# Kernel tuning notes

Measured on AMD Instinct MI355X. Metric: run time of the kernel, lower is better.

## Reference

```python
import jax, jax.numpy as jnp
import numpy as np

K = 4       # wavelet basis size
C = 4       # wavelet channels
ALPHA = 64  # retained Fourier modes per SparseKernelFT
L = 0       # coarsest-level cutoff


def setup_inputs() -> dict:
    key = jax.random.key(0)
    ks = jax.random.split(key, 14)
    B, N = 32, 16384
    ck = C * K
    wscale = 1.0 / (ck * ck)  # matches torch.rand(...)/in_ch^2 scale

    def cw(k1, k2):
        return (jax.random.normal(k1, (ck, ck, ALPHA), jnp.float32) * wscale,
                jax.random.normal(k2, (ck, ck, ALPHA), jnp.float32) * wscale)

    wA_re, wA_im = cw(ks[1], ks[2])
    wB_re, wB_im = cw(ks[3], ks[4])
    wC_re, wC_im = cw(ks[5], ks[6])
    fs = 1.0 / np.sqrt(2.0 * K)  # stand-in scale for orthonormal Legendre filter banks
    return {
        "x": jax.random.normal(ks[0], (B, N, C, K), jnp.float32),
        "ec_s": jax.random.normal(ks[7], (2 * K, K), jnp.float32) * fs,
        "ec_d": jax.random.normal(ks[8], (2 * K, K), jnp.float32) * fs,
        "rc_e": jax.random.normal(ks[9], (2 * K, K), jnp.float32) * fs,
        "rc_o": jax.random.normal(ks[10], (2 * K, K), jnp.float32) * fs,
        "t0_w": jax.random.normal(ks[11], (K, K), jnp.float32) / np.sqrt(K),
        "t0_b": jnp.zeros((K,), jnp.float32),
        "wA_re": wA_re, "wA_im": wA_im,
        "wB_re": wB_re, "wB_im": wB_im,
        "wC_re": wC_re, "wC_im": wC_im,
    }


def _sparse_ft(x, w_re, w_im):
    # SparseKernelFT (1D): rfft -> truncated-mode complex mixing -> irfft.
    B, N, c, k = x.shape
    ck = c * k
    xr = x.reshape(B, N, ck).transpose(0, 2, 1)        # (B, ck, N)
    xf = jnp.fft.rfft(xr)                               # (B, ck, N//2+1)
    nf = N // 2 + 1
    l = min(ALPHA, nf)
    w = (w_re + 1j * w_im)[:, :, :l]                    # (ck, ck, l) complex
    out = jnp.einsum('bix,iox->box', xf[:, :, :l], w)
    out_full = jnp.zeros((B, ck, nf), dtype=out.dtype).at[:, :, :l].set(out)
    y = jnp.fft.irfft(out_full, n=N)                    # real (B, ck, N)
    return y.transpose(0, 2, 1).reshape(B, N, c, k)


def _forward(x, ec_s, ec_d, rc_e, rc_o, t0_w, t0_b,
             wA_re, wA_im, wB_re, wB_im, wC_re, wC_im):
    B, N, c, k = x.shape
    ns = int(np.log2(N))
    Ud, Us = [], []
    # decomposition: N -> N/2 -> ... -> 2^L
    for _ in range(ns - L):
        xa = jnp.concatenate([x[:, ::2], x[:, 1::2]], axis=-1)  # (B, n/2, c, 2k)
        d = xa @ ec_d   # detail coefficients
        x = xa @ ec_s   # scale coefficients
        Ud.append(_sparse_ft(d, wA_re, wA_im) + _sparse_ft(x, wB_re, wB_im))
        Us.append(_sparse_ft(d, wC_re, wC_im))
    # coarsest-scale linear map T0 over last dim k
    x = x @ t0_w.T + t0_b
    # reconstruction with even/odd interleaving
    for i in range(ns - 1 - L, -1, -1):
        x = x + Us[i]
        xc = jnp.concatenate([x, Ud[i]], axis=-1)   # (B, n, c, 2k)
        x_e = xc @ rc_e                              # (B, n, c, k)
        x_o = xc @ rc_o
        b, n = x_e.shape[0], x_e.shape[1]
        x = jnp.stack([x_e, x_o], axis=2).reshape(b, 2 * n, c, k)
    return x


def reference(x, ec_s, ec_d, rc_e, rc_o, t0_w, t0_b,
              wA_re, wA_im, wB_re, wB_im, wC_re, wC_im):
    return _forward(x, ec_s, ec_d, rc_e, rc_o, t0_w, t0_b,
                    wA_re, wA_im, wB_re, wB_im, wC_re, wC_im)
```

## Files before the change

### kernel.cpp

```cpp
#include <hip/hip_runtime.h>

#define TWO_PI 6.28318530717958647692f

constexpr int BB   = 32;
constexpr int NTOT = 16384;
constexpr int CKd  = 16;
constexpr int NLEV = 14;

__device__ __forceinline__ void decomp_row(const float* __restrict__ src,
                                           const float* __restrict__ ec_s,
                                           const float* __restrict__ ec_d,
                                           float* d, float* s)
{
  float xa[32];
#pragma unroll
  for (int q = 0; q < 8; ++q) {
    float4 v = reinterpret_cast<const float4*>(src)[q];
    xa[q*4+0] = v.x; xa[q*4+1] = v.y; xa[q*4+2] = v.z; xa[q*4+3] = v.w;
  }
#pragma unroll
  for (int c = 0; c < 4; ++c) {
#pragma unroll
    for (int j = 0; j < 4; ++j) {
      float ad = 0.f, as = 0.f;
#pragma unroll
      for (int m = 0; m < 4; ++m) {
        const float xe = xa[c*4+m];
        const float xo = xa[16+c*4+m];
        ad += xe * ec_d[m*4+j] + xo * ec_d[(4+m)*4+j];
        as += xe * ec_s[m*4+j] + xo * ec_s[(4+m)*4+j];
      }
      d[c*4+j] = ad; s[c*4+j] = as;
    }
  }
}

__global__ __launch_bounds__(256) void fwd_big(
    const float* __restrict__ xin, float* __restrict__ xout,
    float* __restrict__ Fd, float* __restrict__ Fx,
    const float* __restrict__ ec_s, const float* __restrict__ ec_d,
    int nhalf)
{
  __shared__ float smem[16384];
  float* Pd = smem;
  float* Md = smem + 4096;
  float* Ps = smem + 8192;
  float* Ms = smem + 12288;
  const int b    = blockIdx.x;
  const int t0p  = blockIdx.y << 8;
  const int tid  = threadIdx.x;
  const int halfn = nhalf >> 1;
  const int p    = t0p + tid;

  float da[16], sa[16], db[16], sb[16];
  const size_t rowbase = (size_t)b * (2 * (size_t)nhalf) * CKd;
  decomp_row(xin + rowbase + (2*(size_t)p)*CKd,           ec_s, ec_d, da, sa);
  decomp_row(xin + rowbase + (2*(size_t)(p+halfn))*CKd,   ec_s, ec_d, db, sb);
  {
    float4* o0 = reinterpret_cast<float4*>(xout + ((size_t)b*nhalf + p)*CKd);
    float4* o1 = reinterpret_cast<float4*>(xout + ((size_t)b*nhalf + p + halfn)*CKd);
#pragma unroll
    for (int q = 0; q < 4; ++q) {
      o0[q] = make_float4(sa[q*4], sa[q*4+1], sa[q*4+2], sa[q*4+3]);
      o1[q] = make_float4(sb[q*4], sb[q*4+1], sb[q*4+2], sb[q*4+3]);
    }
  }
#pragma unroll
  for (int i = 0; i < 16; ++i) {
    Pd[tid*16+i] = da[i] + db[i];
    Md[tid*16+i] = da[i] - db[i];
    Ps[tid*16+i] = sa[i] + sb[i];
    Ms[tid*16+i] = sa[i] - sb[i];
  }
  __syncthreads();

  const int f = tid >> 2, g = tid & 3;
  const float* srcd = (f & 1) ? Md : Pd;
  const float* srcs = (f & 1) ? Ms : Ps;
  const int   mask = nhalf - 1;
  const float w    = TWO_PI / (float)nhalf;
  float cv, sv, c1, s1;
  __sincosf((float)((f * t0p) & mask) * w, &sv, &cv);
  __sincosf((float)f * w, &s1, &c1);
  float dre[4] = {0,0,0,0}, dim_[4] = {0,0,0,0};
  float sre[4] = {0,0,0,0}, sim_[4] = {0,0,0,0};
  for (int tt = 0; tt < 256; ++tt) {
    const float4 dv = *reinterpret_cast<const float4*>(srcd + tt*16 + g*4);
    const float4 xv = *reinterpret_cast<const float4*>(srcs + tt*16 + g*4);
    dre[0] += dv.x*cv; dim_[0] -= dv.x*sv;
    dre[1] += dv.y*cv; dim_[1] -= dv.y*sv;
    dre[2] += dv.z*cv; dim_[2] -= dv.z*sv;
    dre[3] += dv.w*cv; dim_[3] -= dv.w*sv;
    sre[0] += xv.x*cv; sim_[0] -= xv.x*sv;
    sre[1] += xv.y*cv; sim_[1] -= xv.y*sv;
    sre[2] += xv.z*cv; sim_[2] -= xv.z*sv;
    sre[3] += xv.w*cv; sim_[3] -= xv.w*sv;
    const float nc = cv*c1 - sv*s1;
    const float ns = sv*c1 + cv*s1;
    cv = nc; sv = ns;
  }
#pragma unroll
  for (int q = 0; q < 4; ++q) {
    const int i = g*4 + q;
    const int base = ((b * CKd + i) * 64 + f) * 2;
    atomicAdd(&Fd[base],   dre[q]);
    atomicAdd(&Fd[base+1], dim_[q]);
    atomicAdd(&Fx[base],   sre[q]);
    atomicAdd(&Fx[base+1], sim_[q]);
  }
}

__global__ void mix_big(
    float* __restrict__ Fd, float* __restrict__ Fx,
    float* __restrict__ G4,
    const float* __restrict__ wAre, const float* __restrict__ wAim,
    const float* __restrict__ wBre, const float* __restrict__ wBim,
    const float* __restrict__ wCre, const float* __restrict__ wCim)
{
  const int b = blockIdx.x;
  const int f = blockIdx.y;
  const int tid = threadIdx.x;
  const int o = tid & 15;
  const bool isUs = tid >= 16;
  float are = 0.f, aim = 0.f;
#pragma unroll 4
  for (int i = 0; i < 16; ++i) {
    const int fb = ((b * CKd + i) * 64 + f) * 2;
    const int wb = (i * CKd + o) * 64 + f;
    const float dre = Fd[fb], dim_ = Fd[fb+1];
    if (!isUs) {
      float wre = wAre[wb], wim = wAim[wb];
      are += dre * wre - dim_ * wim;
      aim += dre * wim + dim_ * wre;
      const float xre = Fx[fb], xim = Fx[fb+1];
      wre = wBre[wb]; wim = wBim[wb];
      are += xre * wre - xim * wim;
      aim += xre * wim + xim * wre;
    } else {
      const float wre = wCre[wb], wim = wCim[wb];
      are += dre * wre - dim_ * wim;
      aim += dre * wim + dim_ * wre;
    }
  }
  float2* gp = reinterpret_cast<float2*>(G4 + ((size_t)(b * CKd + o) * 64 + f) * 4);
  gp[isUs ? 1 : 0] = make_float2(are, aim);
  __syncthreads();
  {
    const int zb = ((b * CKd + o) * 64 + f) * 2;
    float* dst = isUs ? &Fx[zb] : &Fd[zb];
    dst[0] = 0.f; dst[1] = 0.f;
  }
}

__global__ __launch_bounds__(256) void inv_big(
    const float* __restrict__ G4, float* __restrict__ Ud, float* __restrict__ Us,
    int n)
{
  __shared__ float4 gl[64 * 17];
  const int b   = blockIdx.x;
  const int tid = threadIdx.x;
  const float4* Gb = reinterpret_cast<const float4*>(G4) + (size_t)b * 1024;
  for (int s_ = tid; s_ < 1024; s_ += 256) {
    const int i = s_ >> 6, f = s_ & 63;
    float4 v = Gb[(size_t)i * 64 + f];
    if (f) { v.x *= 2.f; v.y *= 2.f; v.z *= 2.f; v.w *= 2.f; }
    gl[f*17 + i] = v;
  }
  __syncthreads();

  const int i   = tid & 15;
  const int col = tid >> 4;
  const int tb  = (blockIdx.y << 6) + col;
  const float w = TWO_PI / (float)n;

  float udE[4], udO[4], usE[4], usO[4], c[4], s[4], c1[4], s1[4];
  {
    const float4 g0 = gl[i];
#pragma unroll
    for (int k = 0; k < 4; ++k) {
      udE[k] = g0.x; usE[k] = g0.z; udO[k] = 0.f; usO[k] = 0.f;
      __sincosf((float)(tb + 16*k) * w, &s1[k], &c1[k]);
      c[k] = c1[k]; s[k] = s1[k];
    }
  }
#pragma unroll 1
  for (int kk = 0; kk < 31; ++kk) {
    {
      const float4 g = gl[(2*kk+1)*17 + i];
#pragma unroll
      for (int k = 0; k < 4; ++k) {
        udO[k] += g.x*c[k] - g.y*s[k];
        usO[k] += g.z*c[k] - g.w*s[k];
        const float nc = c[k]*c1[k] - s[k]*s1[k];
        const float ns = s[k]*c1[k] + c[k]*s1[k];
        c[k] = nc; s[k] = ns;
      }
    }
    {
      const float4 g = gl[(2*kk+2)*17 + i];
#pragma unroll
      for (int k = 0; k < 4; ++k) {
        udE[k] += g.x*c[k] - g.y*s[k];
        usE[k] += g.z*c[k] - g.w*s[k];
        const float nc = c[k]*c1[k] - s[k]*s1[k];
        const float ns = s[k]*c1[k] + c[k]*s1[k];
        c[k] = nc; s[k] = ns;
      }
    }
  }
  {
    const float4 g = gl[63*17 + i];
#pragma unroll
    for (int k = 0; k < 4; ++k) {
      udO[k] += g.x*c[k] - g.y*s[k];
      usO[k] += g.z*c[k] - g.w*s[k];
    }
  }
  const float invn = 1.f / (float)n;
  const int   half = n >> 1;
#pragma unroll
  for (int k = 0; k < 4; ++k) {
    const int t = tb + 16*k;
    const size_t r0 = ((size_t)b*n + t) * CKd + i;
    const size_t r1 = r0 + (size_t)half * CKd;
    Ud[r0] = (udE[k] + udO[k]) * invn;
    Ud[r1] = (udE[k] - udO[k]) * invn;
    Us[r0] = (usE[k] + usO[k]) * invn;
    Us[r1] = (usE[k] - usO[k]) * invn;
  }
}

__global__ __launch_bounds__(256) void fwd_kernel(
    const float* __restrict__ xin, float* __restrict__ xout,
    float* __restrict__ Fd, float* __restrict__ Fx,
    const float* __restrict__ ec_s, const float* __restrict__ ec_d,
    int nhalf, int l)
{
  __shared__ float dt[256][20];
  __shared__ float st[256][20];
  const int b   = blockIdx.x;
  const int t0  = blockIdx.y << 8;
  const int tid = threadIdx.x;
  const int rem = nhalf - t0;
  const int rows = rem < 256 ? rem : 256;
  const int t = t0 + tid;

  if (tid < rows) {
    const float* src = xin + ((size_t)b * (2 * (size_t)nhalf) + 2 * (size_t)t) * CKd;
    float xa[32];
#pragma unroll
    for (int q = 0; q < 8; ++q) {
      float4 v = reinterpret_cast<const float4*>(src)[q];
      xa[q*4+0] = v.x; xa[q*4+1] = v.y; xa[q*4+2] = v.z; xa[q*4+3] = v.w;
    }
    float srow[16];
#pragma unroll
    for (int c = 0; c < 4; ++c) {
#pragma unroll
      for (int j = 0; j < 4; ++j) {
        float ad = 0.f, as = 0.f;
#pragma unroll
        for (int m = 0; m < 4; ++m) {
          const float xe = xa[c*4+m];
          const float xo = xa[16+c*4+m];
          ad += xe * ec_d[m*4+j] + xo * ec_d[(4+m)*4+j];
          as += xe * ec_s[m*4+j] + xo * ec_s[(4+m)*4+j];
        }
        dt[tid][c*4+j] = ad;
        st[tid][c*4+j] = as;
        srow[c*4+j]    = as;
      }
    }
    float4* dst = reinterpret_cast<float4*>(xout + ((size_t)b * nhalf + t) * CKd);
#pragma unroll
    for (int q = 0; q < 4; ++q)
      dst[q] = make_float4(srow[q*4], srow[q*4+1], srow[q*4+2], srow[q*4+3]);
  }
  __syncthreads();

  const int f = tid >> 2, g = tid & 3;
  if (f >= l) return;
  float dre[4] = {0,0,0,0}, dim_[4] = {0,0,0,0};
  float sre[4] = {0,0,0,0}, sim_[4] = {0,0,0,0};
  const int   mask = nhalf - 1;
  const float w    = TWO_PI / (float)nhalf;
  for (int tt = 0; tt < rows; ++tt) {
    const int tg = t0 + tt;
    float sv, cv;
    __sincosf((float)((f * tg) & mask) * w, &sv, &cv);
    const float4 dv = *reinterpret_cast<const float4*>(&dt[tt][g*4]);
    const float4 xv = *reinterpret_cast<const float4*>(&st[tt][g*4]);
    const float dvv[4] = {dv.x, dv.y, dv.z, dv.w};
    const float xvv[4] = {xv.x, xv.y, xv.z, xv.w};
#pragma unroll
    for (int q = 0; q < 4; ++q) {
      dre[q] += dvv[q] * cv;  dim_[q] -= dvv[q] * sv;
      sre[q] += xvv[q] * cv;  sim_[q] -= xvv[q] * sv;
    }
  }
#pragma unroll
  for (int q = 0; q < 4; ++q) {
    const int i = g*4 + q;
    const int base = ((b * CKd + i) * 64 + f) * 2;
    atomicAdd(&Fd[base],   dre[q]);
    atomicAdd(&Fd[base+1], dim_[q]);
    atomicAdd(&Fx[base],   sre[q]);
    atomicAdd(&Fx[base+1], sim_[q]);
  }
}

__global__ void mix_kernel(
    float* __restrict__ Fd, float* __restrict__ Fx,
    float* __restrict__ Gud, float* __restrict__ Gus,
    const float* __restrict__ wAre, const float* __restrict__ wAim,
    const float* __restrict__ wBre, const float* __restrict__ wBim,
    const float* __restrict__ wCre, const float* __restrict__ wCim)
{
  const int b = blockIdx.x;
  const int f = blockIdx.y;
  const int tid = threadIdx.x;
  const int o = tid & 15;
  const bool isUs = tid >= 16;
  float are = 0.f, aim = 0.f;
#pragma unroll 4
  for (int i = 0; i < 16; ++i) {
    const int fb = ((b * CKd + i) * 64 + f) * 2;
    const int wb = (i * CKd + o) * 64 + f;
    const float dre = Fd[fb], dim_ = Fd[fb+1];
    if (!isUs) {
      float wre = wAre[wb], wim = wAim[wb];
      are += dre * wre - dim_ * wim;
      aim += dre * wim + dim_ * wre;
      const float xre = Fx[fb], xim = Fx[fb+1];
      wre = wBre[wb]; wim = wBim[wb];
      are += xre * wre - xim * wim;
      aim += xre * wim + xim * wre;
    } else {
      const float wre = wCre[wb], wim = wCim[wb];
      are += dre * wre - dim_ * wim;
      aim += dre * wim + dim_ * wre;
    }
  }
  const int gb = ((b * CKd + o) * 64 + f) * 2;
  if (!isUs) { Gud[gb] = are; Gud[gb+1] = aim; }
  else       { Gus[gb] = are; Gus[gb+1] = aim; }
  __syncthreads();
  {
    const int zb = ((b * CKd + o) * 64 + f) * 2;
    float* dst = isUs ? &Fx[zb] : &Fd[zb];
    dst[0] = 0.f; dst[1] = 0.f;
  }
}

__global__ __launch_bounds__(256) void inv_kernel(
    const float* __restrict__ Gud, const float* __restrict__ Gus,
    float* __restrict__ Ud, float* __restrict__ Us, int n, int l)
{
  __shared__ float4 sG[64 * 16];
  const int b = blockIdx.x;
  const int tid = threadIdx.x;
  for (int idx = tid; idx < l * 16; idx += 256) {
    const int f = idx >> 4, i = idx & 15;
    const int base = ((b * CKd + i) * 64 + f) * 2;
    sG[idx] = make_float4(Gud[base], Gud[base+1], Gus[base], Gus[base+1]);
  }
  __syncthreads();
  const int t = (blockIdx.y << 8) + tid;
  if (t >= n) return;

  float ud[16], us[16];
#pragma unroll
  for (int i = 0; i < 16; ++i) { const float4 g = sG[i]; ud[i] = g.x; us[i] = g.z; }

  const int   mask = n - 1;
  const float w    = TWO_PI / (float)n;
  for (int f = 1; f < l; ++f) {
    float sv, cv;
    __sincosf((float)((f * t) & mask) * w, &sv, &cv);
    const float scale = (2 * f == n) ? 1.f : 2.f;
    cv *= scale; sv *= scale;
#pragma unroll
    for (int i = 0; i < 16; ++i) {
      const float4 g = sG[f * 16 + i];
      ud[i] += g.x * cv - g.y * sv;
      us[i] += g.z * cv - g.w * sv;
    }
  }
  const float invn = 1.f / (float)n;
  const size_t ro = ((size_t)b * n + t) * CKd;
  float4* pud = reinterpret_cast<float4*>(Ud + ro);
  float4* pus = reinterpret_cast<float4*>(Us + ro);
#pragma unroll
  for (int q = 0; q < 4; ++q) {
    pud[q] = make_float4(ud[q*4]*invn, ud[q*4+1]*invn, ud[q*4+2]*invn, ud[q*4+3]*invn);
    pus[q] = make_float4(us[q*4]*invn, us[q*4+1]*invn, us[q*4+2]*invn, us[q*4+3]*invn);
  }
}

__global__ void t0_kernel(const float* __restrict__ xin, float* __restrict__ xout,
                          const float* __restrict__ t0w, const float* __restrict__ t0b)
{
  const int idx = blockIdx.x * 256 + threadIdx.x;
  if (idx >= BB * CKd) return;
  const int bc = idx >> 2;
  const int k  = idx & 3;
  float acc = t0b[k];
#pragma unroll
  for (int j = 0; j < 4; ++j) acc += xin[bc*4 + j] * t0w[k*4 + j];
  xout[idx] = acc;
}

__global__ __launch_bounds__(256) void recon_kernel(
    const float* __restrict__ xin, const float* __restrict__ UsL,
    const float* __restrict__ UdL, float* __restrict__ xout,
    int n, int lg, const float* __restrict__ rc_e, const float* __restrict__ rc_o)
{
  const int idx = blockIdx.x * 256 + threadIdx.x;
  if (idx >= BB * n) return;
  const int b = idx >> lg;
  const int t = idx & (n - 1);
  const size_t ro = ((size_t)b * n + t) * CKd;
  float xv[16], uv[16], dv[16];
#pragma unroll
  for (int q = 0; q < 4; ++q) {
    const float4 a = reinterpret_cast<const float4*>(xin + ro)[q];
    const float4 u = reinterpret_cast<const float4*>(UsL + ro)[q];
    const float4 d = reinterpret_cast<const float4*>(UdL + ro)[q];
    xv[q*4]=a.x; xv[q*4+1]=a.y; xv[q*4+2]=a.z; xv[q*4+3]=a.w;
    uv[q*4]=u.x; uv[q*4+1]=u.y; uv[q*4+2]=u.z; uv[q*4+3]=u.w;
    dv[q*4]=d.x; dv[q*4+1]=d.y; dv[q*4+2]=d.z; dv[q*4+3]=d.w;
  }
  float xe[16], xo[16];
#pragma unroll
  for (int c = 0; c < 4; ++c) {
    float xc[8];
#pragma unroll
    for (int m = 0; m < 4; ++m) { xc[m] = xv[c*4+m] + uv[c*4+m]; xc[4+m] = dv[c*4+m]; }
#pragma unroll
    for (int k = 0; k < 4; ++k) {
      float ae = 0.f, ao = 0.f;
#pragma unroll
      for (int m = 0; m < 8; ++m) { ae += xc[m] * rc_e[m*4+k]; ao += xc[m] * rc_o[m*4+k]; }
      xe[c*4+k] = ae; xo[c*4+k] = ao;
    }
  }
  float4* out = reinterpret_cast<float4*>(xout + ((size_t)b * (2*(size_t)n) + 2*(size_t)t) * CKd);
#pragma unroll
  for (int q = 0; q < 4; ++q) {
    out[q]   = make_float4(xe[q*4], xe[q*4+1], xe[q*4+2], xe[q*4+3]);
    out[4+q] = make_float4(xo[q*4], xo[q*4+1], xo[q*4+2], xo[q*4+3]);
  }
}

extern "C" void kernel_launch(void* const* d_in, const int* in_sizes, int n_in,
                              void* d_out, int out_size, void* d_ws, size_t ws_size,
                              hipStream_t stream)
{
  const float* x    = (const float*)d_in[0];
  const float* ec_s = (const float*)d_in[1];
  const float* ec_d = (const float*)d_in[2];
  const float* rc_e = (const float*)d_in[3];
  const float* rc_o = (const float*)d_in[4];
  const float* t0w  = (const float*)d_in[5];
  const float* t0b  = (const float*)d_in[6];
  const float* wAre = (const float*)d_in[7];
  const float* wAim = (const float*)d_in[8];
  const float* wBre = (const float*)d_in[9];
  const float* wBim = (const float*)d_in[10];
  const float* wCre = (const float*)d_in[11];
  const float* wCim = (const float*)d_in[12];

  float* ws = (float*)d_ws;
  const size_t XS_ELEMS = (size_t)BB * (NTOT/2) * CKd;
  const size_t U_ELEMS  = (size_t)BB * (NTOT - 1) * CKd;
  const size_t F_ELEMS  = (size_t)BB * CKd * 64 * 2;
  float* xsA = ws;
  float* xsB = xsA + XS_ELEMS;
  float* UdS = xsB + XS_ELEMS;
  float* UsS = UdS + U_ELEMS;
  float* Fd  = UsS + U_ELEMS;
  float* Fx  = Fd + F_ELEMS;
  float* Gud = Fx + F_ELEMS;
  float* Gus = Gud + F_ELEMS;
  float* G4  = Gud;

  float* udl[NLEV]; float* usl[NLEV]; int nlv[NLEV];

  hipMemsetAsync(Fd, 0, 2 * F_ELEMS * sizeof(float), stream);

  const float* cur = x;
  float* nxt = xsA;
  size_t uoff = 0;
  int nhalf = NTOT / 2;
  for (int j = 0; j < NLEV; ++j, nhalf >>= 1) {
    const int l = (nhalf/2 + 1 < 64) ? (nhalf/2 + 1) : 64;
    udl[j] = UdS + uoff; usl[j] = UsS + uoff; nlv[j] = nhalf;
    if (nhalf >= 512) {
      fwd_big<<<dim3(BB, nhalf/512), 256, 0, stream>>>(cur, nxt, Fd, Fx, ec_s, ec_d, nhalf);
      mix_big<<<dim3(BB, 64), 32, 0, stream>>>(Fd, Fx, G4,
                                               wAre, wAim, wBre, wBim, wCre, wCim);
      inv_big<<<dim3(BB, nhalf/128), 256, 0, stream>>>(G4, udl[j], usl[j], nhalf);
    } else {
      const int S = (nhalf + 255) / 256;
      fwd_kernel<<<dim3(BB, S), 256, 0, stream>>>(cur, nxt, Fd, Fx, ec_s, ec_d, nhalf, l);
      mix_kernel<<<dim3(BB, l), 32, 0, stream>>>(Fd, Fx, Gud, Gus,
                                                 wAre, wAim, wBre, wBim, wCre, wCim);
      inv_kernel<<<dim3(BB, S), 256, 0, stream>>>(Gud, Gus, udl[j], usl[j], nhalf, l);
    }
    uoff += (size_t)BB * nhalf * CKd;
    cur = nxt;
    nxt = (nxt == xsA) ? xsB : xsA;
  }

  t0_kernel<<<2, 256, 0, stream>>>(cur, nxt, t0w, t0b);
  cur = nxt;
  nxt = (nxt == xsA) ? xsB : xsA;

  for (int i = NLEV - 1; i >= 0; --i) {
    const int n = nlv[i];
    int lg = 0; while ((1 << lg) < n) ++lg;
    float* out = (i == 0) ? (float*)d_out : nxt;
    const int total = BB * n;
    recon_kernel<<<(total + 255) / 256, 256, 0, stream>>>(cur, usl[i], udl[i], out,
                                                          n, lg, rc_e, rc_o);
    cur = out;
    nxt = (nxt == xsA) ? xsB : xsA;
  }
}
```

Before: 680.1 us.

## Unify spectral mixing into one per-batch kernel and widen inverse DFT tiles

Replaces the per-frequency 32-thread mix kernels with a single 256-thread-per-batch mix kernel that reads weights and spectra as float4 and computes all three complex mixes per thread, writing a packed G4 layout. The small-level inverse kernel now reads the same packed layout. inv_big processes 8 time columns per thread with a software-prefetched shared-memory load, halving its grid. The intent is to cut launch overhead, improve memory coalescing and raise ILP, at the cost of higher register pressure in inv_big.

Result: slower. 712.6 us (+4.8%).

```diff
diff --git a/kernel.cpp b/kernel.cpp
--- a/kernel.cpp
+++ b/kernel.cpp
@@ -110,45 +110,68 @@
   }
 }
 
-__global__ void mix_big(
+__global__ __launch_bounds__(256) void mix2_kernel(
     float* __restrict__ Fd, float* __restrict__ Fx,
     float* __restrict__ G4,
     const float* __restrict__ wAre, const float* __restrict__ wAim,
     const float* __restrict__ wBre, const float* __restrict__ wBim,
     const float* __restrict__ wCre, const float* __restrict__ wCim)
 {
-  const int b = blockIdx.x;
-  const int f = blockIdx.y;
+  const int b  = blockIdx.x;
   const int tid = threadIdx.x;
-  const int o = tid & 15;
-  const bool isUs = tid >= 16;
-  float are = 0.f, aim = 0.f;
-#pragma unroll 4
+  const int o  = tid >> 4;
+  const int fs = tid & 15;
+
+  const float4* Fd4 = reinterpret_cast<const float4*>(Fd);
+  const float4* Fx4 = reinterpret_cast<const float4*>(Fx);
+
+  float udre[4] = {0,0,0,0}, udim[4] = {0,0,0,0};
+  float usre[4] = {0,0,0,0}, usim[4] = {0,0,0,0};
+
+#pragma unroll 2
   for (int i = 0; i < 16; ++i) {
-    const int fb = ((b * CKd + i) * 64 + f) * 2;
-    const int wb = (i * CKd + o) * 64 + f;
-    const float dre = Fd[fb], dim_ = Fd[fb+1];
-    if (!isUs) {
-      float wre = wAre[wb], wim = wAim[wb];
-      are += dre * wre - dim_ * wim;
-      aim += dre * wim + dim_ * wre;
-      const float xre = Fx[fb], xim = Fx[fb+1];
-      wre = wBre[wb]; wim = wBim[wb];
-      are += xre * wre - xim * wim;
-      aim += xre * wim + xim * wre;
-    } else {
-      const float wre = wCre[wb], wim = wCim[wb];
-      are += dre * wre - dim_ * wim;
-      aim += dre * wim + dim_ * wre;
-    }
-  }
-  float2* gp = reinterpret_cast<float2*>(G4 + ((size_t)(b * CKd + o) * 64 + f) * 4);
-  gp[isUs ? 1 : 0] = make_float2(are, aim);
+    const int wb4 = (i*16 + o)*16 + fs;
+    const float4 war = reinterpret_cast<const float4*>(wAre)[wb4];
+    const float4 wai = reinterpret_cast<const float4*>(wAim)[wb4];
+    const float4 wbr = reinterpret_cast<const float4*>(wBre)[wb4];
+    const float4 wbi = reinterpret_cast<const float4*>(wBim)[wb4];
+    const float4 wcr = reinterpret_cast<const float4*>(wCre)[wb4];
+    const float4 wci = reinterpret_cast<const float4*>(wCim)[wb4];
+    const int fb4 = (b*16 + i)*32 + 2*fs;
+    const float4 d01 = Fd4[fb4], d23 = Fd4[fb4+1];
+    const float4 x01 = Fx4[fb4], x23 = Fx4[fb4+1];
+
+    const float fdre[4] = {d01.x, d01.z, d23.x, d23.z};
+    const float fdim[4] = {d01.y, d01.w, d23.y, d23.w};
+    const float fxre[4] = {x01.x, x01.z, x23.x, x23.z};
+    const float fxim[4] = {x01.y, x01.w, x23.y, x23.w};
+    const float ware[4] = {war.x, war.y, war.z, war.w};
+    const float waim[4] = {wai.x, wai.y, wai.z, wai.w};
+    const float wbre[4] = {wbr.x, wbr.y, wbr.z, wbr.w};
+    const float wbim[4] = {wbi.x, wbi.y, wbi.z, wbi.w};
+    const float wcre[4] = {wcr.x, wcr.y, wcr.z, wcr.w};
+    const float wcim[4] = {wci.x, wci.y, wci.z, wci.w};
+#pragma unroll
+    for (int j = 0; j < 4; ++j) {
+      udre[j] += fdre[j]*ware[j] - fdim[j]*waim[j] + fxre[j]*wbre[j] - fxim[j]*wbim[j];
+      udim[j] += fdre[j]*waim[j] + fdim[j]*ware[j] + fxre[j]*wbim[j] + fxim[j]*wbre[j];
+      usre[j] += fdre[j]*wcre[j] - fdim[j]*wcim[j];
+      usim[j] += fdre[j]*wcim[j] + fdim[j]*wcre[j];
+    }
+  }
+  float4* G4f = reinterpret_cast<float4*>(G4);
+#pragma unroll
+  for (int j = 0; j < 4; ++j)
+    G4f[(b*16 + o)*64 + 4*fs + j] = make_float4(udre[j], udim[j], usre[j], usim[j]);
+
   __syncthreads();
   {
-    const int zb = ((b * CKd + o) * 64 + f) * 2;
-    float* dst = isUs ? &Fx[zb] : &Fd[zb];
-    dst[0] = 0.f; dst[1] = 0.f;
+    float4* Fdw = reinterpret_cast<float4*>(Fd);
+    float4* Fxw = reinterpret_cast<float4*>(Fx);
+    const int fb4 = (b*16 + o)*32 + 2*fs;
+    const float4 z = make_float4(0.f, 0.f, 0.f, 0.f);
+    Fdw[fb4] = z; Fdw[fb4+1] = z;
+    Fxw[fb4] = z; Fxw[fb4+1] = z;
   }
 }
 
@@ -168,59 +191,54 @@
   }
   __syncthreads();
 
-  const int i   = tid & 15;
-  const int col = tid >> 4;
-  const int tb  = (blockIdx.y << 6) + col;
-  const float w = TWO_PI / (float)n;
-
-  float udE[4], udO[4], usE[4], usO[4], c[4], s[4], c1[4], s1[4];
+  const int i    = tid & 15;
+  const int col  = tid >> 4;
+  const int base = blockIdx.y << 7;
+  const float w  = TWO_PI / (float)n;
+
+  float udE[8], udO[8], usE[8], usO[8], c[8], s[8], c1[8], s1[8];
   {
     const float4 g0 = gl[i];
 #pragma unroll
-    for (int k = 0; k < 4; ++k) {
+    for (int k = 0; k < 8; ++k) {
       udE[k] = g0.x; usE[k] = g0.z; udO[k] = 0.f; usO[k] = 0.f;
-      __sincosf((float)(tb + 16*k) * w, &s1[k], &c1[k]);
+      __sincosf((float)(base + col + 16*k) * w, &s1[k], &c1[k]);
       c[k] = c1[k]; s[k] = s1[k];
     }
   }
+  float4 ga = gl[17 + i];
 #pragma unroll 1
   for (int kk = 0; kk < 31; ++kk) {
-    {
-      const float4 g = gl[(2*kk+1)*17 + i];
-#pragma unroll
-      for (int k = 0; k < 4; ++k) {
-        udO[k] += g.x*c[k] - g.y*s[k];
-        usO[k] += g.z*c[k] - g.w*s[k];
-        const float nc = c[k]*c1[k] - s[k]*s1[k];
-        const float ns = s[k]*c1[k] + c[k]*s1[k];
-        c[k] = nc; s[k] = ns;
-      }
-    }
-    {
-      const float4 g = gl[(2*kk+2)*17 + i];
-#pragma unroll
-      for (int k = 0; k < 4; ++k) {
-        udE[k] += g.x*c[k] - g.y*s[k];
-        usE[k] += g.z*c[k] - g.w*s[k];
-        const float nc = c[k]*c1[k] - s[k]*s1[k];
-        const float ns = s[k]*c1[k] + c[k]*s1[k];
-        c[k] = nc; s[k] = ns;
-      }
-    }
-  }
-  {
-    const float4 g = gl[63*17 + i];
-#pragma unroll
-    for (int k = 0; k < 4; ++k) {
-      udO[k] += g.x*c[k] - g.y*s[k];
-      usO[k] += g.z*c[k] - g.w*s[k];
-    }
+    const float4 gb = gl[(2*kk+2)*17 + i];
+#pragma unroll
+    for (int k = 0; k < 8; ++k) {
+      udO[k] += ga.x*c[k] - ga.y*s[k];
+      usO[k] += ga.z*c[k] - ga.w*s[k];
+      const float nc = c[k]*c1[k] - s[k]*s1[k];
+      const float ns = s[k]*c1[k] + c[k]*s1[k];
+      c[k] = nc; s[k] = ns;
+    }
+    const float4 gn = gl[(2*kk+3)*17 + i];
+#pragma unroll
+    for (int k = 0; k < 8; ++k) {
+      udE[k] += gb.x*c[k] - gb.y*s[k];
+      usE[k] += gb.z*c[k] - gb.w*s[k];
+      const float nc = c[k]*c1[k] - s[k]*s1[k];
+      const float ns = s[k]*c1[k] + c[k]*s1[k];
+      c[k] = nc; s[k] = ns;
+    }
+    ga = gn;
+  }
+#pragma unroll
+  for (int k = 0; k < 8; ++k) {
+    udO[k] += ga.x*c[k] - ga.y*s[k];
+    usO[k] += ga.z*c[k] - ga.w*s[k];
   }
   const float invn = 1.f / (float)n;
   const int   half = n >> 1;
 #pragma unroll
-  for (int k = 0; k < 4; ++k) {
-    const int t = tb + 16*k;
+  for (int k = 0; k < 8; ++k) {
+    const int t = base + col + 16*k;
     const size_t r0 = ((size_t)b*n + t) * CKd + i;
     const size_t r1 = r0 + (size_t)half * CKd;
     Ud[r0] = (udE[k] + udO[k]) * invn;
@@ -309,60 +327,17 @@
   }
 }
 
-__global__ void mix_kernel(
-    float* __restrict__ Fd, float* __restrict__ Fx,
-    float* __restrict__ Gud, float* __restrict__ Gus,
-    const float* __restrict__ wAre, const float* __restrict__ wAim,
-    const float* __restrict__ wBre, const float* __restrict__ wBim,
-    const float* __restrict__ wCre, const float* __restrict__ wCim)
-{
-  const int b = blockIdx.x;
-  const int f = blockIdx.y;
-  const int tid = threadIdx.x;
-  const int o = tid & 15;
-  const bool isUs = tid >= 16;
-  float are = 0.f, aim = 0.f;
-#pragma unroll 4
-  for (int i = 0; i < 16; ++i) {
-    const int fb = ((b * CKd + i) * 64 + f) * 2;
-    const int wb = (i * CKd + o) * 64 + f;
-    const float dre = Fd[fb], dim_ = Fd[fb+1];
-    if (!isUs) {
-      float wre = wAre[wb], wim = wAim[wb];
-      are += dre * wre - dim_ * wim;
-      aim += dre * wim + dim_ * wre;
-      const float xre = Fx[fb], xim = Fx[fb+1];
-      wre = wBre[wb]; wim = wBim[wb];
-      are += xre * wre - xim * wim;
-      aim += xre * wim + xim * wre;
-    } else {
-      const float wre = wCre[wb], wim = wCim[wb];
-      are += dre * wre - dim_ * wim;
-      aim += dre * wim + dim_ * wre;
-    }
-  }
-  const int gb = ((b * CKd + o) * 64 + f) * 2;
-  if (!isUs) { Gud[gb] = are; Gud[gb+1] = aim; }
-  else       { Gus[gb] = are; Gus[gb+1] = aim; }
-  __syncthreads();
-  {
-    const int zb = ((b * CKd + o) * 64 + f) * 2;
-    float* dst = isUs ? &Fx[zb] : &Fd[zb];
-    dst[0] = 0.f; dst[1] = 0.f;
-  }
-}
-
 __global__ __launch_bounds__(256) void inv_kernel(
-    const float* __restrict__ Gud, const float* __restrict__ Gus,
+    const float* __restrict__ G4,
     float* __restrict__ Ud, float* __restrict__ Us, int n, int l)
 {
   __shared__ float4 sG[64 * 16];
   const int b = blockIdx.x;
   const int tid = threadIdx.x;
-  for (int idx = tid; idx < l * 16; idx += 256) {
-    const int f = idx >> 4, i = idx & 15;
-    const int base = ((b * CKd + i) * 64 + f) * 2;
-    sG[idx] = make_float4(Gud[base], Gud[base+1], Gus[base], Gus[base+1]);
+  const float4* Gb = reinterpret_cast<const float4*>(G4) + (size_t)b * 1024;
+  for (int s_ = tid; s_ < 1024; s_ += 256) {
+    const int i = s_ >> 6, f = s_ & 63;
+    if (f < l) sG[f*16 + i] = Gb[(size_t)i * 64 + f];
   }
   __syncthreads();
   const int t = (blockIdx.y << 8) + tid;
@@ -480,9 +455,7 @@
   float* UsS = UdS + U_ELEMS;
   float* Fd  = UsS + U_ELEMS;
   float* Fx  = Fd + F_ELEMS;
-  float* Gud = Fx + F_ELEMS;
-  float* Gus = Gud + F_ELEMS;
-  float* G4  = Gud;
+  float* G4  = Fx + F_ELEMS;
 
   float* udl[NLEV]; float* usl[NLEV]; int nlv[NLEV];
 
@@ -497,15 +470,14 @@
     udl[j] = UdS + uoff; usl[j] = UsS + uoff; nlv[j] = nhalf;
     if (nhalf >= 512) {
       fwd_big<<<dim3(BB, nhalf/512), 256, 0, stream>>>(cur, nxt, Fd, Fx, ec_s, ec_d, nhalf);
-      mix_big<<<dim3(BB, 64), 32, 0, stream>>>(Fd, Fx, G4,
-                                               wAre, wAim, wBre, wBim, wCre, wCim);
-      inv_big<<<dim3(BB, nhalf/128), 256, 0, stream>>>(G4, udl[j], usl[j], nhalf);
+      mix2_kernel<<<BB, 256, 0, stream>>>(Fd, Fx, G4,
+                                          wAre, wAim, wBre, wBim, wCre, wCim);
+      inv_big<<<dim3(BB, nhalf/256), 256, 0, stream>>>(G4, udl[j], usl[j], nhalf);
     } else {
-      const int S = (nhalf + 255) / 256;
-      fwd_kernel<<<dim3(BB, S), 256, 0, stream>>>(cur, nxt, Fd, Fx, ec_s, ec_d, nhalf, l);
-      mix_kernel<<<dim3(BB, l), 32, 0, stream>>>(Fd, Fx, Gud, Gus,
-                                                 wAre, wAim, wBre, wBim, wCre, wCim);
-      inv_kernel<<<dim3(BB, S), 256, 0, stream>>>(Gud, Gus, udl[j], usl[j], nhalf, l);
+      fwd_kernel<<<dim3(BB, 1), 256, 0, stream>>>(cur, nxt, Fd, Fx, ec_s, ec_d, nhalf, l);
+      mix2_kernel<<<BB, 256, 0, stream>>>(Fd, Fx, G4,
+                                          wAre, wAim, wBre, wBim, wCre, wCim);
+      inv_kernel<<<dim3(BB, 1), 256, 0, stream>>>(G4, udl[j], usl[j], nhalf, l);
     }
     uoff += (size_t)BB * nhalf * CKd;
     cur = nxt;
```
